# Performance work log

Measured on AMD Instinct MI355X. Metric: run time of the kernel, lower is better.

Reference implementation:

```python
import jax, jax.numpy as jnp
import numpy as np

B = 1024          # batch
IN_FEATURES = 20000
N_GROUP = 64
G_IN = 512        # indices gathered per group
H1 = 256          # first Linear out dim per group
GROUP_SIZE = 128  # second Linear out dim per group


def setup_inputs() -> dict:
    key = jax.random.key(0)
    k_x, k_idx, k_w1, k_b1, k_w2, k_b2 = jax.random.split(key, 6)
    x = jax.random.normal(k_x, (B, IN_FEATURES), dtype=jnp.float32)
    idx = jax.random.randint(k_idx, (N_GROUP, G_IN), 0, IN_FEATURES, dtype=jnp.int64)
    # Stacked per-group Linear weights (uniform group shapes allow batching).
    s1 = 1.0 / np.sqrt(G_IN)
    s2 = 1.0 / np.sqrt(H1)
    W1 = jax.random.uniform(k_w1, (N_GROUP, G_IN, H1), jnp.float32, -s1, s1)
    b1 = jax.random.uniform(k_b1, (N_GROUP, H1), jnp.float32, -s1, s1)
    W2 = jax.random.uniform(k_w2, (N_GROUP, H1, GROUP_SIZE), jnp.float32, -s2, s2)
    b2 = jax.random.uniform(k_b2, (N_GROUP, GROUP_SIZE), jnp.float32, -s2, s2)
    return {"x": x, "idx": idx, "W1": W1, "b1": b1, "W2": W2, "b2": b2}


def reference(x, idx, W1, b1, W2, b2):
    # Per-group gather of input columns: [B, n_group, G_IN]
    g = x[:, idx]
    # Two bare Linears per group (no activation, matching the source Sequential).
    h = jnp.einsum('bgi,gio->bgo', g, W1) + b1          # [B, n_group, H1]
    o = jnp.einsum('bgh,gho->bgo', h, W2) + b2          # [B, n_group, GROUP_SIZE]
    # Concat groups along feature dim -> [B, n_group*GROUP_SIZE]
    return o.reshape(o.shape[0], -1)
```

## Files before the change

### kernel.cpp

```cpp
#include <hip/hip_runtime.h>
#include <hip/hip_bf16.h>
#include <stdint.h>


typedef __attribute__((ext_vector_type(4))) float f32x4;
typedef __attribute__((ext_vector_type(8))) __bf16 bf16x8;
typedef __attribute__((ext_vector_type(8))) uint16_t u16x8;

__device__ __forceinline__ uint16_t f2bf(float f) {
    uint32_t u = __float_as_uint(f);
    u += 0x7FFFu + ((u >> 16) & 1u);
    return (uint16_t)(u >> 16);
}

__device__ __forceinline__ uint64_t pack4bf(f32x4 v) {
    return (uint64_t)f2bf(v[0]) | ((uint64_t)f2bf(v[1]) << 16)
         | ((uint64_t)f2bf(v[2]) << 32) | ((uint64_t)f2bf(v[3]) << 48);
}

__global__ __launch_bounds__(1024, 8) void k_prep(const float* __restrict__ x,
                                                  const int* __restrict__ idx,
                                                  const float* __restrict__ W1,
                                                  const float* __restrict__ b1,
                                                  const float* __restrict__ W2,
                                                  const float* __restrict__ b2,
                                                  uint16_t* __restrict__ Wc,
                                                  float* __restrict__ bias2,
                                                  uint32_t* __restrict__ G32) {
    __shared__ __align__(16) uint8_t smem[81920];
    const int bid = blockIdx.x;
    const int t = threadIdx.x;

    if (bid < 256) {
        uint16_t* As = (uint16_t*)smem;
        uint16_t* Bs = As + 5120;
        const int g = bid >> 2, mt = bid & 3;
        const int wid = t >> 6, l = t & 63;
        const int wm = wid >> 2, wn = wid & 3;
        const int q = l >> 4, lm = l & 15;
        const float* W1g = W1 + ((size_t)g * 512 + (size_t)mt * 128) * 256;
        const float* W2g = W2 + (size_t)g * 256 * 128;
        f32x4 acc[2][2];
        #pragma unroll
        for (int mi = 0; mi < 2; ++mi)
            #pragma unroll
            for (int ni = 0; ni < 2; ++ni) {
                f32x4 z = {0.f, 0.f, 0.f, 0.f};
                acc[mi][ni] = z;
            }
        for (int kt = 0; kt < 8; ++kt) {
            __syncthreads();
            {
                int m = t >> 3, c4 = t & 7;
                f32x4 v = *(const f32x4*)(W1g + (size_t)m * 256 + kt * 32 + c4 * 4);
                *(uint64_t*)&As[m * 40 + c4 * 4] = pack4bf(v);
            }
            {
                int h = t >> 5, n4 = t & 31;
                f32x4 v = *(const f32x4*)(W2g + (size_t)(kt * 32 + h) * 128 + n4 * 4);
                *(uint64_t*)&Bs[h * 132 + n4 * 4] = pack4bf(v);
            }
            __syncthreads();
            bf16x8 a[2];
            #pragma unroll
            for (int mi = 0; mi < 2; ++mi)
                a[mi] = *(const bf16x8*)&As[(wm * 32 + mi * 16 + lm) * 40 + q * 8];
            #pragma unroll
            for (int ni = 0; ni < 2; ++ni) {
                int n = wn * 32 + ni * 16 + lm;
                u16x8 bu;
                #pragma unroll
                for (int j = 0; j < 8; ++j) bu[j] = Bs[(q * 8 + j) * 132 + n];
                bf16x8 bv = __builtin_bit_cast(bf16x8, bu);
                #pragma unroll
                for (int mi = 0; mi < 2; ++mi)
                    acc[mi][ni] = __builtin_amdgcn_mfma_f32_16x16x32_bf16(a[mi], bv, acc[mi][ni], 0, 0, 0);
            }
        }
        uint16_t* Wcg = Wc + (size_t)g * 128 * 512;
        #pragma unroll
        for (int mi = 0; mi < 2; ++mi) {
            int k0 = mt * 128 + wm * 32 + mi * 16 + q * 4;
            #pragma unroll
            for (int ni = 0; ni < 2; ++ni) {
                int n = wn * 32 + ni * 16 + lm;
                *(uint64_t*)&Wcg[(size_t)n * 512 + k0] = pack4bf(acc[mi][ni]);
            }
        }
    } else if (bid < 320) {
        if (t < 128) {
            const int g = bid - 256, n = t;
            const float* w = W2 + (size_t)g * 256 * 128 + n;
            const float* bb = b1 + g * 256;
            float s = b2[g * 128 + n];
            for (int h = 0; h < 256; ++h) s += bb[h] * w[(size_t)h * 128];
            bias2[g * 128 + n] = s;
        }
    } else {
        float* shf = (float*)smem;
        const int b = bid - 320;
        const float* xrow = x + (size_t)b * 20000;
        const int wb = (t >> 6) << 6;
        #pragma unroll
        for (int i = 0; i < 5; ++i) {
            int c = t + i * 1024;
            int csrc = c < 5000 ? c : 4999;
            __builtin_amdgcn_global_load_lds(
                (const __attribute__((address_space(1))) void*)(xrow + (size_t)csrc * 4),
                (__attribute__((address_space(3))) void*)(shf + (size_t)(wb + i * 1024) * 4),
                16, 0, 0);
        }
        __syncthreads();
        const int4* idx4 = (const int4*)idx;
        int4 nv = idx4[t];
        #pragma unroll
        for (int it = 0; it < 8; ++it) {
            int4 cv = nv;
            if (it < 7) nv = idx4[t + (it + 1) * 1024];
            float f0 = shf[cv.x], f1 = shf[cv.y], f2 = shf[cv.z], f3 = shf[cv.w];
            uint32_t w0, w1;
            asm("v_cvt_pk_bf16_f32 %0, %1, %2" : "=v"(w0) : "v"(f0), "v"(f1));
            asm("v_cvt_pk_bf16_f32 %0, %1, %2" : "=v"(w1) : "v"(f2), "v"(f3));
            int j = t + it * 1024;
            int g = j >> 7, kd = j & 127;
            uint2 p; p.x = w0; p.y = w1;
            *(uint2*)&G32[(size_t)g * 262144 + (size_t)b * 256 + kd * 2] = p;
        }
    }
}

__global__ __launch_bounds__(256) void k_gemm(const uint16_t* __restrict__ G,
                                              const uint16_t* __restrict__ Wc,
                                              const float* __restrict__ bias2,
                                              float* __restrict__ out) {
    __shared__ uint16_t sh[16384];
    uint16_t* As = sh;
    uint16_t* Bs = sh + 8192;
    const int wg = (blockIdx.x & 7) * 64 + (blockIdx.x >> 3);
    const int g = wg >> 3, mt = wg & 7;
    const int t = threadIdx.x;
    const int wid = t >> 6, l = t & 63;
    const int wm = wid >> 1, wn = wid & 1;
    const int q = l >> 4, lm = l & 15;
    const int lrow = l >> 3;
    const int lcolsw = ((l & 7) ^ lrow) * 8;
    const uint16_t* Ga = G + (size_t)g * 524288 + (size_t)mt * 128 * 512;
    const uint16_t* Wa = Wc + (size_t)g * 65536;

    f32x4 acc[4][4];
    #pragma unroll
    for (int mi = 0; mi < 4; ++mi)
        #pragma unroll
        for (int ni = 0; ni < 4; ++ni) {
            f32x4 z = {0.f, 0.f, 0.f, 0.f};
            acc[mi][ni] = z;
        }

    for (int kt = 0; kt < 8; ++kt) {
        __syncthreads();
        #pragma unroll
        for (int r = 0; r < 4; ++r) {
            const int rowbase = wid * 8 + r * 32;
            const uint16_t* sA = Ga + (size_t)(rowbase + lrow) * 512 + kt * 64 + lcolsw;
            const uint16_t* sB = Wa + (size_t)(rowbase + lrow) * 512 + kt * 64 + lcolsw;
            __builtin_amdgcn_global_load_lds(
                (const __attribute__((address_space(1))) void*)sA,
                (__attribute__((address_space(3))) void*)(As + rowbase * 64), 16, 0, 0);
            __builtin_amdgcn_global_load_lds(
                (const __attribute__((address_space(1))) void*)sB,
                (__attribute__((address_space(3))) void*)(Bs + rowbase * 64), 16, 0, 0);
        }
        __syncthreads();
        #pragma unroll
        for (int kk = 0; kk < 2; ++kk) {
            bf16x8 a[4], b[4];
            #pragma unroll
            for (int mi = 0; mi < 4; ++mi) {
                int row = wm * 64 + mi * 16 + lm;
                int off = row * 64 + ((kk * 32 + q * 8) ^ ((lm & 7) * 8));
                a[mi] = *(const bf16x8*)&As[off];
            }
            #pragma unroll
            for (int ni = 0; ni < 4; ++ni) {
                int row = wn * 64 + ni * 16 + lm;
                int off = row * 64 + ((kk * 32 + q * 8) ^ ((lm & 7) * 8));
                b[ni] = *(const bf16x8*)&Bs[off];
            }
            #pragma unroll
            for (int mi = 0; mi < 4; ++mi)
                #pragma unroll
                for (int ni = 0; ni < 4; ++ni)
                    acc[mi][ni] = __builtin_amdgcn_mfma_f32_16x16x32_bf16(a[mi], b[ni], acc[mi][ni], 0, 0, 0);
        }
    }
    float bn[4];
    #pragma unroll
    for (int ni = 0; ni < 4; ++ni) bn[ni] = bias2[g * 128 + wn * 64 + ni * 16 + lm];
    #pragma unroll
    for (int mi = 0; mi < 4; ++mi)
        #pragma unroll
        for (int ni = 0; ni < 4; ++ni) {
            int col = g * 128 + wn * 64 + ni * 16 + lm;
            #pragma unroll
            for (int r = 0; r < 4; ++r) {
                int brow = mt * 128 + wm * 64 + mi * 16 + q * 4 + r;
                out[(size_t)brow * 8192 + col] = acc[mi][ni][r] + bn[ni];
            }
        }
}

extern "C" void kernel_launch(void* const* d_in, const int* in_sizes, int n_in,
                              void* d_out, int out_size, void* d_ws, size_t ws_size,
                              hipStream_t stream) {
    (void)in_sizes; (void)n_in; (void)out_size; (void)ws_size;
    const float* x   = (const float*)d_in[0];
    const int*   idx = (const int*)d_in[1];
    const float* W1  = (const float*)d_in[2];
    const float* b1  = (const float*)d_in[3];
    const float* W2  = (const float*)d_in[4];
    const float* b2  = (const float*)d_in[5];
    float* out = (float*)d_out;

    uint16_t* G     = (uint16_t*)d_ws;
    uint16_t* Wc    = (uint16_t*)((char*)d_ws + (size_t)(64 << 20));
    float*    bias2 = (float*)   ((char*)d_ws + (size_t)(72 << 20));

    k_prep<<<1344, 1024, 0, stream>>>(x, idx, W1, b1, W2, b2, Wc, bias2, (uint32_t*)G);
    k_gemm<<<512,  256, 0, stream>>>(G, Wc, bias2, out);
}
```

Before: 58.31 us.

## Split prep into weight and gather kernels with double-buffered multi-row gather

Splits the fused prep kernel into a weight/bias kernel and a separate gather kernel. Each gather block now handles four batch rows, double-buffering the x-row loads into LDS so the next row's load overlaps the current row's gather. The block also loads the idx vectors into registers once and reuses them across the four rows. In exchange it adds a third sequential launch and loses the overlap between weight prep and gather. It also uses the full 160KB of LDS, so only one gather block fits per CU.

```diff
diff --git a/kernel.cpp b/kernel.cpp
--- a/kernel.cpp
+++ b/kernel.cpp
@@ -18,16 +18,13 @@
          | ((uint64_t)f2bf(v[2]) << 32) | ((uint64_t)f2bf(v[3]) << 48);
 }
 
-__global__ __launch_bounds__(1024, 8) void k_prep(const float* __restrict__ x,
-                                                  const int* __restrict__ idx,
-                                                  const float* __restrict__ W1,
-                                                  const float* __restrict__ b1,
-                                                  const float* __restrict__ W2,
-                                                  const float* __restrict__ b2,
-                                                  uint16_t* __restrict__ Wc,
-                                                  float* __restrict__ bias2,
-                                                  uint32_t* __restrict__ G32) {
-    __shared__ __align__(16) uint8_t smem[81920];
+__global__ __launch_bounds__(1024) void k_wb(const float* __restrict__ W1,
+                                             const float* __restrict__ b1,
+                                             const float* __restrict__ W2,
+                                             const float* __restrict__ b2,
+                                             uint16_t* __restrict__ Wc,
+                                             float* __restrict__ bias2) {
+    __shared__ __align__(16) uint8_t smem[18688];
     const int bid = blockIdx.x;
     const int t = threadIdx.x;
 
@@ -87,7 +84,7 @@
                 *(uint64_t*)&Wcg[(size_t)n * 512 + k0] = pack4bf(acc[mi][ni]);
             }
         }
-    } else if (bid < 320) {
+    } else {
         if (t < 128) {
             const int g = bid - 256, n = t;
             const float* w = W2 + (size_t)g * 256 * 128 + n;
@@ -96,28 +93,64 @@
             for (int h = 0; h < 256; ++h) s += bb[h] * w[(size_t)h * 128];
             bias2[g * 128 + n] = s;
         }
-    } else {
-        float* shf = (float*)smem;
-        const int b = bid - 320;
-        const float* xrow = x + (size_t)b * 20000;
-        const int wb = (t >> 6) << 6;
+    }
+}
+
+__global__ __launch_bounds__(1024, 4) void k_gather(const float* __restrict__ x,
+                                                    const int* __restrict__ idx,
+                                                    uint32_t* __restrict__ G32) {
+    extern __shared__ float shf[];
+    const int t = threadIdx.x;
+    const int wb = (t >> 6) << 6;
+    const int b0 = blockIdx.x * 4;
+
+    const int4* idx4 = (const int4*)idx;
+    int4 iv0 = idx4[t];
+    int4 iv1 = idx4[t + 1024];
+    int4 iv2 = idx4[t + 2048];
+    int4 iv3 = idx4[t + 3072];
+    int4 iv4 = idx4[t + 4096];
+    int4 iv5 = idx4[t + 5120];
+    int4 iv6 = idx4[t + 6144];
+    int4 iv7 = idx4[t + 7168];
+
+    {
+        const float* xr = x + (size_t)b0 * 20000;
         #pragma unroll
         for (int i = 0; i < 5; ++i) {
             int c = t + i * 1024;
             int csrc = c < 5000 ? c : 4999;
             __builtin_amdgcn_global_load_lds(
-                (const __attribute__((address_space(1))) void*)(xrow + (size_t)csrc * 4),
+                (const __attribute__((address_space(1))) void*)(xr + (size_t)csrc * 4),
                 (__attribute__((address_space(3))) void*)(shf + (size_t)(wb + i * 1024) * 4),
                 16, 0, 0);
         }
-        __syncthreads();
-        const int4* idx4 = (const int4*)idx;
-        int4 nv = idx4[t];
+    }
+    __syncthreads();
+
+    #pragma unroll
+    for (int r = 0; r < 4; ++r) {
+        const float* cur = shf + (size_t)(r & 1) * 20480;
+        float* nxt = shf + (size_t)((r + 1) & 1) * 20480;
+        if (r < 3) {
+            const float* xr = x + (size_t)(b0 + r + 1) * 20000;
+            #pragma unroll
+            for (int i = 0; i < 5; ++i) {
+                int c = t + i * 1024;
+                int csrc = c < 5000 ? c : 4999;
+                __builtin_amdgcn_global_load_lds(
+                    (const __attribute__((address_space(1))) void*)(xr + (size_t)csrc * 4),
+                    (__attribute__((address_space(3))) void*)(nxt + (size_t)(wb + i * 1024) * 4),
+                    16, 0, 0);
+            }
+        }
+        __builtin_amdgcn_sched_barrier(0);
+        const int b = b0 + r;
         #pragma unroll
         for (int it = 0; it < 8; ++it) {
-            int4 cv = nv;
-            if (it < 7) nv = idx4[t + (it + 1) * 1024];
-            float f0 = shf[cv.x], f1 = shf[cv.y], f2 = shf[cv.z], f3 = shf[cv.w];
+            int4 cv = it == 0 ? iv0 : it == 1 ? iv1 : it == 2 ? iv2 : it == 3 ? iv3
+                    : it == 4 ? iv4 : it == 5 ? iv5 : it == 6 ? iv6 : iv7;
+            float f0 = cur[cv.x], f1 = cur[cv.y], f2 = cur[cv.z], f3 = cur[cv.w];
             uint32_t w0, w1;
             asm("v_cvt_pk_bf16_f32 %0, %1, %2" : "=v"(w0) : "v"(f0), "v"(f1));
             asm("v_cvt_pk_bf16_f32 %0, %1, %2" : "=v"(w1) : "v"(f2), "v"(f3));
@@ -126,6 +159,7 @@
             uint2 p; p.x = w0; p.y = w1;
             *(uint2*)&G32[(size_t)g * 262144 + (size_t)b * 256 + kd * 2] = p;
         }
+        __syncthreads();
     }
 }
 
@@ -225,6 +259,7 @@
     uint16_t* Wc    = (uint16_t*)((char*)d_ws + (size_t)(64 << 20));
     float*    bias2 = (float*)   ((char*)d_ws + (size_t)(72 << 20));
 
-    k_prep<<<1344, 1024, 0, stream>>>(x, idx, W1, b1, W2, b2, Wc, bias2, (uint32_t*)G);
-    k_gemm<<<512,  256, 0, stream>>>(G, Wc, bias2, out);
-}
+    k_wb    <<<320, 1024, 0, stream>>>(W1, b1, W2, b2, Wc, bias2);
+    k_gather<<<256, 1024, 163840, stream>>>(x, idx, (uint32_t*)G);
+    k_gemm  <<<512,  256, 0, stream>>>(G, Wc, bias2, out);
+}
```

After: 60.78 us. +4.2%, slower.
